# Kernel tuning notes

Hardware: AMD Instinct MI355X
Metric: run time of the kernel (lower is better)

## Reference

```python
import jax, jax.numpy as jnp
import numpy as np

B, T, N, E, F = 8, 12, 20000, 320000, 64  # batch, timedim, nodes, edges, gcn hidden


def setup_inputs() -> dict:
    key = jax.random.key(0)
    ks = jax.random.split(key, 8)
    x = jax.random.normal(ks[0], (B, T, N), dtype=jnp.float32)
    edge_src = jax.random.randint(ks[1], (E,), 0, N, dtype=jnp.int32)
    edge_dst = jax.random.randint(ks[2], (E,), 0, N, dtype=jnp.int32)
    # pre-normalized GCN adjacency values (spektral expects D^-1/2 (A+I) D^-1/2)
    edge_weight = jax.random.uniform(ks[3], (E,), dtype=jnp.float32)
    w_gcn = jax.random.normal(ks[4], (T, F), dtype=jnp.float32) * (1.0 / np.sqrt(T))
    b_gcn = jnp.zeros((F,), dtype=jnp.float32)
    w_dense = jax.random.normal(ks[5], (F, T), dtype=jnp.float32) * (1.0 / np.sqrt(F))
    b_dense = jnp.zeros((T,), dtype=jnp.float32)
    return {"x": x, "edge_weight": edge_weight, "w_gcn": w_gcn, "b_gcn": b_gcn,
            "w_dense": w_dense, "b_dense": b_dense,
            "edge_src": edge_src, "edge_dst": edge_dst}


def reference(x, edge_weight, w_gcn, b_gcn, w_dense, b_dense, edge_src, edge_dst):
    # x: [B, T, N] -> transpose to [B, N, T] (nodes x features), as in call()
    xt = jnp.transpose(x, (0, 2, 1))                      # [B, N, T]
    # GCNConv: relu(A @ (X @ W) + b)
    h = jnp.einsum("bnt,tf->bnf", xt, w_gcn)              # [B, N, F]
    msg = h[:, edge_src, :] * edge_weight[None, :, None]  # [B, E, F] gather * edge value
    agg = jnp.zeros_like(h).at[:, edge_dst, :].add(msg)   # scatter-add (SpMM)
    gcn = jax.nn.relu(agg + b_gcn)                        # [B, N, F]
    # SFDense: relu(gcn @ Wd + bd) -> [B, N, T]
    return jax.nn.relu(jnp.einsum("bnf,ft->bnt", gcn, w_dense) + b_dense)
```

## Files before the change

kernel.cpp:

```cpp
#include <hip/hip_runtime.h>

#define BB 8
#define TT 12
#define NN 20000
#define EE 320000
#define FF 64
#define NC 96
#define NU 48
#define CAP 64

__device__ __forceinline__ unsigned int f2bf(float v) {
    unsigned int u = __float_as_uint(v);
    return (u + 0x7FFFu + ((u >> 16) & 1u)) >> 16;
}

__global__ __launch_bounds__(256) void prep_kernel(const float* __restrict__ x,
                                                   unsigned int* __restrict__ xt,
                                                   int* __restrict__ cnt) {
    int n = blockIdx.x * 256 + threadIdx.x;
    if (n >= NN) return;
    cnt[n] = 0;
    unsigned int* row = xt + (size_t)n * NU;
#pragma unroll
    for (int b = 0; b < BB; ++b) {
        float v[TT];
#pragma unroll
        for (int t = 0; t < TT; ++t)
            v[t] = x[((size_t)(b * TT + t)) * NN + n];
        unsigned int u[6];
#pragma unroll
        for (int j = 0; j < 6; ++j)
            u[j] = f2bf(v[2 * j]) | (f2bf(v[2 * j + 1]) << 16);
        uint2* o = reinterpret_cast<uint2*>(row + b * 6);
        o[0] = make_uint2(u[0], u[1]);
        o[1] = make_uint2(u[2], u[3]);
        o[2] = make_uint2(u[4], u[5]);
    }
}

__global__ void build_kernel(const int* __restrict__ esrc, const int* __restrict__ edst,
                             const float* __restrict__ ew,
                             int* __restrict__ cnt, int2* __restrict__ csrf) {
    int e = blockIdx.x * blockDim.x + threadIdx.x;
    if (e >= EE) return;
    int d = edst[e];
    int slot = atomicAdd(&cnt[d], 1);
    if (slot < CAP)
        csrf[(size_t)d * CAP + slot] = make_int2(esrc[e], __float_as_int(ew[e]));
}

__global__ __launch_bounds__(256) void agg_kernel(const unsigned int* __restrict__ xt,
                                                  const int* __restrict__ cnt,
                                                  const int2* __restrict__ csrf,
                                                  float* __restrict__ agg) {
    int lane = threadIdx.x & 63;
    int n = (blockIdx.x * blockDim.x + threadIdx.x) >> 6;
    if (n >= NN) return;
    int jend = min(cnt[n], CAP);
    const int2* row = csrf + (size_t)n * CAP;
    bool act = lane < NU;
    int li = act ? lane : (lane - 16);
    float a0 = 0.f, a1 = 0.f;
    int j = 0;
    for (; j + 4 <= jend; j += 4) {
        int2 e0 = row[j], e1 = row[j + 1], e2 = row[j + 2], e3 = row[j + 3];
        unsigned int v0 = xt[(size_t)e0.x * NU + li];
        unsigned int v1 = xt[(size_t)e1.x * NU + li];
        unsigned int v2 = xt[(size_t)e2.x * NU + li];
        unsigned int v3 = xt[(size_t)e3.x * NU + li];
        float w0 = __int_as_float(e0.y), w1 = __int_as_float(e1.y);
        float w2 = __int_as_float(e2.y), w3 = __int_as_float(e3.y);
        a0 = fmaf(w0, __uint_as_float(v0 << 16), a0);
        a1 = fmaf(w0, __uint_as_float(v0 & 0xFFFF0000u), a1);
        a0 = fmaf(w1, __uint_as_float(v1 << 16), a0);
        a1 = fmaf(w1, __uint_as_float(v1 & 0xFFFF0000u), a1);
        a0 = fmaf(w2, __uint_as_float(v2 << 16), a0);
        a1 = fmaf(w2, __uint_as_float(v2 & 0xFFFF0000u), a1);
        a0 = fmaf(w3, __uint_as_float(v3 << 16), a0);
        a1 = fmaf(w3, __uint_as_float(v3 & 0xFFFF0000u), a1);
    }
    for (; j < jend; ++j) {
        int2 e0 = row[j];
        unsigned int v0 = xt[(size_t)e0.x * NU + li];
        float w0 = __int_as_float(e0.y);
        a0 = fmaf(w0, __uint_as_float(v0 << 16), a0);
        a1 = fmaf(w0, __uint_as_float(v0 & 0xFFFF0000u), a1);
    }
    if (act) {
        float2* o = reinterpret_cast<float2*>(agg + (size_t)n * NC + 2 * lane);
        *o = make_float2(a0, a1);
    }
}

__global__ __launch_bounds__(256) void dense_kernel(
        const float* __restrict__ agg,
        const float* __restrict__ wg,
        const float* __restrict__ bg,
        const float* __restrict__ wd,
        const float* __restrict__ bd,
        float* __restrict__ out) {
    __shared__ __align__(16) float s_wgT[FF * TT];
    __shared__ __align__(16) float s_wd[FF * TT];
    __shared__ float s_bg[FF];
    __shared__ float s_bd[TT];
    for (int i = threadIdx.x; i < FF * TT; i += 256) {
        int t = i / FF, f = i % FF;
        s_wgT[f * TT + t] = wg[i];
        s_wd[i] = wd[i];
    }
    if (threadIdx.x < FF) s_bg[threadIdx.x] = bg[threadIdx.x];
    if (threadIdx.x < TT) s_bd[threadIdx.x] = bd[threadIdx.x];
    __syncthreads();

    int b  = threadIdx.x >> 5;
    int nl = threadIdx.x & 31;
    int n = blockIdx.x * 32 + nl;
    if (n >= NN) return;

    float yr[TT];
    const float4* ar = reinterpret_cast<const float4*>(agg + (size_t)n * NC + b * TT);
    float4 a = ar[0], c = ar[1], d4 = ar[2];
    yr[0] = a.x;  yr[1] = a.y;  yr[2]  = a.z;  yr[3]  = a.w;
    yr[4] = c.x;  yr[5] = c.y;  yr[6]  = c.z;  yr[7]  = c.w;
    yr[8] = d4.x; yr[9] = d4.y; yr[10] = d4.z; yr[11] = d4.w;

    float o[TT];
#pragma unroll
    for (int t = 0; t < TT; ++t) o[t] = s_bd[t];

#pragma unroll 8
    for (int f = 0; f < FF; ++f) {
        const float4* wgr = reinterpret_cast<const float4*>(&s_wgT[f * TT]);
        float4 g0 = wgr[0], g1 = wgr[1], g2 = wgr[2];
        float acc = s_bg[f];
        acc += yr[0] * g0.x + yr[1] * g0.y + yr[2] * g0.z + yr[3] * g0.w;
        acc += yr[4] * g1.x + yr[5] * g1.y + yr[6] * g1.z + yr[7] * g1.w;
        acc += yr[8] * g2.x + yr[9] * g2.y + yr[10] * g2.z + yr[11] * g2.w;
        float g = fmaxf(acc, 0.f);
        const float4* wdr = reinterpret_cast<const float4*>(&s_wd[f * TT]);
        float4 d0 = wdr[0], d1 = wdr[1], d2 = wdr[2];
        o[0] += g * d0.x;  o[1] += g * d0.y;  o[2]  += g * d0.z;  o[3]  += g * d0.w;
        o[4] += g * d1.x;  o[5] += g * d1.y;  o[6]  += g * d1.z;  o[7]  += g * d1.w;
        o[8] += g * d2.x;  o[9] += g * d2.y;  o[10] += g * d2.z;  o[11] += g * d2.w;
    }

    float4* op = reinterpret_cast<float4*>(out + ((size_t)b * NN + n) * TT);
    op[0] = make_float4(fmaxf(o[0], 0.f), fmaxf(o[1], 0.f), fmaxf(o[2], 0.f), fmaxf(o[3], 0.f));
    op[1] = make_float4(fmaxf(o[4], 0.f), fmaxf(o[5], 0.f), fmaxf(o[6], 0.f), fmaxf(o[7], 0.f));
    op[2] = make_float4(fmaxf(o[8], 0.f), fmaxf(o[9], 0.f), fmaxf(o[10], 0.f), fmaxf(o[11], 0.f));
}

extern "C" void kernel_launch(void* const* d_in, const int* in_sizes, int n_in,
                              void* d_out, int out_size, void* d_ws, size_t ws_size,
                              hipStream_t stream) {
    const float* x    = (const float*)d_in[0];
    const float* ew   = (const float*)d_in[1];
    const float* wg   = (const float*)d_in[2];
    const float* bg   = (const float*)d_in[3];
    const float* wd   = (const float*)d_in[4];
    const float* bd   = (const float*)d_in[5];
    const int*   esrc = (const int*)d_in[6];
    const int*   edst = (const int*)d_in[7];
    float* out = (float*)d_out;

    unsigned int* xt  = (unsigned int*)d_ws;
    float* agg  = (float*)(xt + (size_t)NN * NU);
    int2*  csrf = (int2*)(agg + (size_t)NN * NC);
    int*   cnt  = (int*)(csrf + (size_t)NN * CAP);

    prep_kernel<<<(NN + 255) / 256, 256, 0, stream>>>(x, xt, cnt);
    build_kernel<<<(EE + 255) / 256, 256, 0, stream>>>(esrc, edst, ew, cnt, csrf);
    agg_kernel<<<(NN * 64 + 255) / 256, 256, 0, stream>>>(xt, cnt, csrf, agg);
    dense_kernel<<<(NN + 31) / 32, 256, 0, stream>>>(agg, wg, bg, wd, bd, out);
}
```

Baseline: 134.1 us.

## Merge prep and build kernels and process four nodes per thread in dense

Result: no change. 134.6 us (+0.4%).

```diff
diff --git a/kernel.cpp b/kernel.cpp
--- a/kernel.cpp
+++ b/kernel.cpp
@@ -9,44 +9,46 @@
 #define NU 48
 #define CAP 64
 
+#define PREP_BLOCKS ((NN + 255) / 256)
+#define BUILD_BLOCKS ((EE + 255) / 256)
+
 __device__ __forceinline__ unsigned int f2bf(float v) {
     unsigned int u = __float_as_uint(v);
     return (u + 0x7FFFu + ((u >> 16) & 1u)) >> 16;
 }
 
-__global__ __launch_bounds__(256) void prep_kernel(const float* __restrict__ x,
-                                                   unsigned int* __restrict__ xt,
-                                                   int* __restrict__ cnt) {
-    int n = blockIdx.x * 256 + threadIdx.x;
-    if (n >= NN) return;
-    cnt[n] = 0;
-    unsigned int* row = xt + (size_t)n * NU;
-#pragma unroll
-    for (int b = 0; b < BB; ++b) {
-        float v[TT];
-#pragma unroll
-        for (int t = 0; t < TT; ++t)
-            v[t] = x[((size_t)(b * TT + t)) * NN + n];
-        unsigned int u[6];
-#pragma unroll
-        for (int j = 0; j < 6; ++j)
-            u[j] = f2bf(v[2 * j]) | (f2bf(v[2 * j + 1]) << 16);
-        uint2* o = reinterpret_cast<uint2*>(row + b * 6);
-        o[0] = make_uint2(u[0], u[1]);
-        o[1] = make_uint2(u[2], u[3]);
-        o[2] = make_uint2(u[4], u[5]);
-    }
-}
-
-__global__ void build_kernel(const int* __restrict__ esrc, const int* __restrict__ edst,
-                             const float* __restrict__ ew,
-                             int* __restrict__ cnt, int2* __restrict__ csrf) {
-    int e = blockIdx.x * blockDim.x + threadIdx.x;
-    if (e >= EE) return;
-    int d = edst[e];
-    int slot = atomicAdd(&cnt[d], 1);
-    if (slot < CAP)
-        csrf[(size_t)d * CAP + slot] = make_int2(esrc[e], __float_as_int(ew[e]));
+__global__ __launch_bounds__(256) void prep_build_kernel(
+        const float* __restrict__ x, unsigned int* __restrict__ xt,
+        const int* __restrict__ esrc, const int* __restrict__ edst,
+        const float* __restrict__ ew,
+        int* __restrict__ cnt, int2* __restrict__ csrf) {
+    if (blockIdx.x < PREP_BLOCKS) {
+        int n = blockIdx.x * 256 + threadIdx.x;
+        if (n >= NN) return;
+        unsigned int* row = xt + (size_t)n * NU;
+#pragma unroll
+        for (int b = 0; b < BB; ++b) {
+            float v[TT];
+#pragma unroll
+            for (int t = 0; t < TT; ++t)
+                v[t] = x[((size_t)(b * TT + t)) * NN + n];
+            unsigned int u[6];
+#pragma unroll
+            for (int j = 0; j < 6; ++j)
+                u[j] = f2bf(v[2 * j]) | (f2bf(v[2 * j + 1]) << 16);
+            uint2* o = reinterpret_cast<uint2*>(row + b * 6);
+            o[0] = make_uint2(u[0], u[1]);
+            o[1] = make_uint2(u[2], u[3]);
+            o[2] = make_uint2(u[4], u[5]);
+        }
+    } else {
+        int e = (blockIdx.x - PREP_BLOCKS) * 256 + threadIdx.x;
+        if (e >= EE) return;
+        int d = edst[e];
+        int slot = atomicAdd(&cnt[d], 1);
+        if ((unsigned)slot < CAP)
+            csrf[(size_t)d * CAP + slot] = make_int2(esrc[e], __float_as_int(ew[e]));
+    }
 }
 
 __global__ __launch_bounds__(256) void agg_kernel(const unsigned int* __restrict__ xt,
@@ -92,6 +94,7 @@
     }
 }
 
+#define KN 4
 __global__ __launch_bounds__(256) void dense_kernel(
         const float* __restrict__ agg,
         const float* __restrict__ wg,
@@ -114,40 +117,63 @@
 
     int b  = threadIdx.x >> 5;
     int nl = threadIdx.x & 31;
-    int n = blockIdx.x * 32 + nl;
-    if (n >= NN) return;
-
-    float yr[TT];
-    const float4* ar = reinterpret_cast<const float4*>(agg + (size_t)n * NC + b * TT);
-    float4 a = ar[0], c = ar[1], d4 = ar[2];
-    yr[0] = a.x;  yr[1] = a.y;  yr[2]  = a.z;  yr[3]  = a.w;
-    yr[4] = c.x;  yr[5] = c.y;  yr[6]  = c.z;  yr[7]  = c.w;
-    yr[8] = d4.x; yr[9] = d4.y; yr[10] = d4.z; yr[11] = d4.w;
-
-    float o[TT];
-#pragma unroll
-    for (int t = 0; t < TT; ++t) o[t] = s_bd[t];
+    int n0 = blockIdx.x * (32 * KN) + nl * KN;
+
+    float yr[KN][TT];
+    int nv = 0;
+#pragma unroll
+    for (int k = 0; k < KN; ++k) {
+        int n = n0 + k;
+        if (n < NN) {
+            const float4* ar = reinterpret_cast<const float4*>(agg + (size_t)n * NC + b * TT);
+            float4 a = ar[0], c = ar[1], d4 = ar[2];
+            yr[k][0] = a.x;  yr[k][1] = a.y;  yr[k][2]  = a.z;  yr[k][3]  = a.w;
+            yr[k][4] = c.x;  yr[k][5] = c.y;  yr[k][6]  = c.z;  yr[k][7]  = c.w;
+            yr[k][8] = d4.x; yr[k][9] = d4.y; yr[k][10] = d4.z; yr[k][11] = d4.w;
+            nv = k + 1;
+        } else {
+#pragma unroll
+            for (int t = 0; t < TT; ++t) yr[k][t] = 0.f;
+        }
+    }
+
+    float o[KN][TT];
+#pragma unroll
+    for (int k = 0; k < KN; ++k)
+#pragma unroll
+        for (int t = 0; t < TT; ++t) o[k][t] = s_bd[t];
 
 #pragma unroll 8
     for (int f = 0; f < FF; ++f) {
         const float4* wgr = reinterpret_cast<const float4*>(&s_wgT[f * TT]);
         float4 g0 = wgr[0], g1 = wgr[1], g2 = wgr[2];
-        float acc = s_bg[f];
-        acc += yr[0] * g0.x + yr[1] * g0.y + yr[2] * g0.z + yr[3] * g0.w;
-        acc += yr[4] * g1.x + yr[5] * g1.y + yr[6] * g1.z + yr[7] * g1.w;
-        acc += yr[8] * g2.x + yr[9] * g2.y + yr[10] * g2.z + yr[11] * g2.w;
-        float g = fmaxf(acc, 0.f);
         const float4* wdr = reinterpret_cast<const float4*>(&s_wd[f * TT]);
         float4 d0 = wdr[0], d1 = wdr[1], d2 = wdr[2];
-        o[0] += g * d0.x;  o[1] += g * d0.y;  o[2]  += g * d0.z;  o[3]  += g * d0.w;
-        o[4] += g * d1.x;  o[5] += g * d1.y;  o[6]  += g * d1.z;  o[7]  += g * d1.w;
-        o[8] += g * d2.x;  o[9] += g * d2.y;  o[10] += g * d2.z;  o[11] += g * d2.w;
-    }
-
-    float4* op = reinterpret_cast<float4*>(out + ((size_t)b * NN + n) * TT);
-    op[0] = make_float4(fmaxf(o[0], 0.f), fmaxf(o[1], 0.f), fmaxf(o[2], 0.f), fmaxf(o[3], 0.f));
-    op[1] = make_float4(fmaxf(o[4], 0.f), fmaxf(o[5], 0.f), fmaxf(o[6], 0.f), fmaxf(o[7], 0.f));
-    op[2] = make_float4(fmaxf(o[8], 0.f), fmaxf(o[9], 0.f), fmaxf(o[10], 0.f), fmaxf(o[11], 0.f));
+        float bgf = s_bg[f];
+#pragma unroll
+        for (int k = 0; k < KN; ++k) {
+            float acc = bgf;
+            acc += yr[k][0] * g0.x + yr[k][1] * g0.y + yr[k][2]  * g0.z + yr[k][3]  * g0.w;
+            acc += yr[k][4] * g1.x + yr[k][5] * g1.y + yr[k][6]  * g1.z + yr[k][7]  * g1.w;
+            acc += yr[k][8] * g2.x + yr[k][9] * g2.y + yr[k][10] * g2.z + yr[k][11] * g2.w;
+            float g = fmaxf(acc, 0.f);
+            o[k][0] += g * d0.x;  o[k][1] += g * d0.y;  o[k][2]  += g * d0.z;  o[k][3]  += g * d0.w;
+            o[k][4] += g * d1.x;  o[k][5] += g * d1.y;  o[k][6]  += g * d1.z;  o[k][7]  += g * d1.w;
+            o[k][8] += g * d2.x;  o[k][9] += g * d2.y;  o[k][10] += g * d2.z;  o[k][11] += g * d2.w;
+        }
+    }
+
+#pragma unroll
+    for (int k = 0; k < KN; ++k) {
+        if (k >= nv) break;
+        float4* op = reinterpret_cast<float4*>(out + ((size_t)b * NN + (n0 + k)) * TT);
+        op[0] = make_float4(fmaxf(o[k][0], 0.f), fmaxf(o[k][1], 0.f),
+                            fmaxf(o[k][2], 0.f), fmaxf(o[k][3], 0.f));
+        op[1] = make_float4(fmaxf(o[k][4], 0.f), fmaxf(o[k][5], 0.f),
+                            fmaxf(o[k][6], 0.f), fmaxf(o[k][7], 0.f));
+        op[2] = make_float4(fmaxf(o[k][8], 0.f), fmaxf(o[k][9], 0.f),
+                            fmaxf(o[k][10], 0.f), fmaxf(o[k][11], 0.f));
+    }
 }
 
 extern "C" void kernel_launch(void* const* d_in, const int* in_sizes, int n_in,
@@ -168,8 +194,9 @@
     int2*  csrf = (int2*)(agg + (size_t)NN * NC);
     int*   cnt  = (int*)(csrf + (size_t)NN * CAP);
 
-    prep_kernel<<<(NN + 255) / 256, 256, 0, stream>>>(x, xt, cnt);
-    build_kernel<<<(EE + 255) / 256, 256, 0, stream>>>(esrc, edst, ew, cnt, csrf);
+    hipMemsetAsync(cnt, 0, NN * sizeof(int), stream);
+    prep_build_kernel<<<PREP_BLOCKS + BUILD_BLOCKS, 256, 0, stream>>>(
+        x, xt, esrc, edst, ew, cnt, csrf);
     agg_kernel<<<(NN * 64 + 255) / 256, 256, 0, stream>>>(xt, cnt, csrf, agg);
-    dense_kernel<<<(NN + 31) / 32, 256, 0, stream>>>(agg, wg, bg, wd, bd, out);
-}
+    dense_kernel<<<(NN + 32 * KN - 1) / (32 * KN), 256, 0, stream>>>(agg, wg, bg, wd, bd, out);
+}
```
